# Optimization experiments

Measured on AMD Instinct MI355X. Metric: run time of the kernel, lower is better.

## Reference

```python
import jax, jax.numpy as jnp
import numpy as np

N = 100000        # num_nodes
W_IN = 256        # input feature dim
W_OUT = 64        # args.node_dim
C = 2             # args.num_channels
T = 4             # num_edge_type
E = 800000        # edges per edge type
NUM_CLASS = 4
M = 20000         # number of target nodes
BETA = 0.5        # args.beta


def setup_inputs() -> dict:
    key = jax.random.key(0)
    ks = jax.random.split(key, 10)
    X = jax.random.normal(ks[0], (N, W_IN), dtype=jnp.float32)
    edge_index = jax.random.randint(ks[1], (T, 2, E), 0, N)
    edge_value = jax.random.uniform(ks[2], (T, E), dtype=jnp.float32)
    target_x = jax.random.randint(ks[3], (M,), 0, N)
    target = jax.random.randint(ks[4], (M,), 0, NUM_CLASS)
    # learned params
    Ws = jax.random.normal(ks[5], (C, W_IN, W_OUT), dtype=jnp.float32) * 0.05   # GCNConv weights
    conv_weight = jax.random.normal(ks[6], (C, T), dtype=jnp.float32) * 0.1     # FastGTConv.weight
    linear1_W = jax.random.normal(ks[7], (W_OUT, W_OUT * C), dtype=jnp.float32) * 0.05
    linear1_b = jnp.zeros((W_OUT,), dtype=jnp.float32)
    lin_W = jax.random.normal(ks[8], (NUM_CLASS, W_OUT), dtype=jnp.float32) * 0.05
    lin_b = jnp.zeros((NUM_CLASS,), dtype=jnp.float32)
    return dict(X=X, edge_value=edge_value, Ws=Ws, conv_weight=conv_weight,
                linear1_W=linear1_W, linear1_b=linear1_b, lin_W=lin_W, lin_b=lin_b,
                edge_index=edge_index, target_x=target_x, target=target)


def reference(X, edge_value, Ws, conv_weight, linear1_W, linear1_b, lin_W, lin_b,
              edge_index, target_x, target):
    # FastGTConv: softmax over edge types per channel
    filt = jax.nn.softmax(conv_weight, axis=1)            # [C, T]
    rows = edge_index[:, 0, :].reshape(-1)                # [T*E]
    cols = edge_index[:, 1, :].reshape(-1)                # [T*E]
    # X_ = H = [X @ W_c for each channel]
    X_ = jnp.einsum('nd,cdo->cno', X, Ws)                 # [C, N, W_OUT]
    outs = []
    for c in range(C):
        # concat+coalesce(add) then spmm == scatter-add of weighted messages
        vals = (edge_value * filt[c][:, None]).reshape(-1)       # [T*E]
        msgs = vals[:, None] * X_[c][cols]                        # [T*E, W_OUT]
        Hc = jax.ops.segment_sum(msgs, rows, num_segments=N)      # [N, W_OUT]
        outs.append(jax.nn.relu(BETA * X_[c] + (1.0 - BETA) * Hc))
    H_ = jnp.concatenate(outs, axis=1)                    # [N, C*W_OUT]
    H_ = jax.nn.relu(H_ @ linear1_W.T + linear1_b)        # [N, W_OUT]
    y = H_[target_x] @ lin_W.T + lin_b                    # [M, NUM_CLASS]
    logp = jax.nn.log_softmax(y, axis=-1)
    loss = -jnp.mean(jnp.take_along_axis(logp, target[:, None], axis=1))
    return loss, y
```

## Files before the change

### kernel.cpp

```cpp
#include <hip/hip_runtime.h>

#define N_NODES 100000
#define W_INF   256
#define W_OUTF  64
#define C_CH    2
#define T_ET    4
#define E_EDGE  800000
#define NUM_CLS 4
#define M_TGT   20000
#define BETA    0.5f
#define MAXDEG  96

typedef __attribute__((ext_vector_type(8))) short bf16x8;
typedef __attribute__((ext_vector_type(4))) float floatx4;

__device__ inline short f2bf(float f) {
    unsigned u = __builtin_bit_cast(unsigned, f);
    u += 0x7FFF + ((u >> 16) & 1);
    return (short)(u >> 16);
}
__device__ inline float bflo(unsigned q) { return __builtin_bit_cast(float, q << 16); }
__device__ inline float bfhi(unsigned q) { return __builtin_bit_cast(float, q & 0xFFFF0000u); }
__device__ __forceinline__ float rlane(float v, int k) {
    return __builtin_bit_cast(float,
        __builtin_amdgcn_readlane(__builtin_bit_cast(int, v), k));
}

__global__ void setup_kernel(const float* __restrict__ Ws,
                             const float* __restrict__ conv_weight,
                             const int* __restrict__ target_x,
                             short* __restrict__ Bt, float* __restrict__ filt,
                             int* __restrict__ rid, int* __restrict__ nrows,
                             float* __restrict__ out) {
    int i = blockIdx.x * 256 + threadIdx.x;
    if (i == 0) { nrows[0] = 0; out[0] = 0.f; }
    if (i < C_CH) {
        int c = i;
        float mx = -1e30f;
        for (int t = 0; t < T_ET; t++) mx = fmaxf(mx, conv_weight[c * T_ET + t]);
        float e[T_ET];
        float s = 0.f;
        for (int t = 0; t < T_ET; t++) { e[t] = expf(conv_weight[c * T_ET + t] - mx); s += e[t]; }
        for (int t = 0; t < T_ET; t++) filt[c * T_ET + t] = e[t] / s;
    }
    if (i < C_CH * W_OUTF * W_INF) {
        int co = i >> 8, k = i & 255;
        int c = co >> 6, o = co & 63;
        Bt[i] = f2bf(Ws[((size_t)c * W_INF + k) * W_OUTF + o]);
    }
    if (i < M_TGT) rid[target_x[i]] = -2;
}

__global__ void compact_kernel(int* __restrict__ rid, int* __restrict__ row_list,
                               int* __restrict__ nrows, int* __restrict__ counts) {
    int n = blockIdx.x * blockDim.x + threadIdx.x;
    if (n < M_TGT) counts[n] = 0;
    int lane = threadIdx.x & 63;
    bool flag = (n < N_NODES) && (rid[n] == -2);
    unsigned long long mask = __ballot(flag);
    int base = 0;
    if (lane == 0 && mask) base = atomicAdd(nrows, __popcll(mask));
    base = __shfl(base, 0);
    if (flag) {
        int id = base + __popcll(mask & ((1ULL << lane) - 1ULL));
        rid[n] = id;
        row_list[id] = n;
    }
}

#define GMT  64
#define BLDA2 136
#define GEMM_NB  ((N_NODES + GMT - 1) / GMT)
#define BUILD_BX ((E_EDGE / 8 + 255) / 256)
#define BUILD_TOT (BUILD_BX * T_ET)
__global__ __launch_bounds__(256, 4)
void fused_gemm_build(const float* __restrict__ X, const short* __restrict__ Bt,
                      short* __restrict__ Xp,
                      const int* __restrict__ edge_index,
                      const float* __restrict__ edge_value,
                      const float* __restrict__ filt,
                      const int* __restrict__ rid,
                      int* __restrict__ counts,
                      unsigned long long* __restrict__ records) {
    __shared__ short Bl[64][BLDA2];
    int tid = threadIdx.x;
    int bx = blockIdx.x;
    if ((bx & 1) == 0) {
        int g = bx >> 1;
        if (g >= GEMM_NB) return;
        int w = tid >> 6, lane = tid & 63;
        int quad = lane >> 4, l15 = lane & 15;
        int m0 = g * GMT + w * 16;
        int arow = m0 + l15;
        if (arow >= N_NODES) arow = N_NODES - 1;
        const float* xrow = X + (size_t)arow * W_INF;
        floatx4 acc[C_CH][4] = {};
        #pragma unroll 1
        for (int kh = 0; kh < 2; kh++) {
            bf16x8 af[4];
            #pragma unroll
            for (int kc = 0; kc < 4; kc++) {
                int kb = kh * 128 + kc * 32 + quad * 8;
                float4 v0 = *(const float4*)&xrow[kb];
                float4 v1 = *(const float4*)&xrow[kb + 4];
                af[kc][0] = f2bf(v0.x); af[kc][1] = f2bf(v0.y);
                af[kc][2] = f2bf(v0.z); af[kc][3] = f2bf(v0.w);
                af[kc][4] = f2bf(v1.x); af[kc][5] = f2bf(v1.y);
                af[kc][6] = f2bf(v1.z); af[kc][7] = f2bf(v1.w);
            }
            #pragma unroll
            for (int c = 0; c < C_CH; c++) {
                if (kh | c) __syncthreads();
                #pragma unroll
                for (int l = 0; l < 4; l++) {
                    int idx = tid + l * 256;
                    int r = idx >> 4;
                    int kp = (idx & 15) * 8;
                    *(bf16x8*)&Bl[r][kp] =
                        *(const bf16x8*)&Bt[(size_t)(c * 64 + r) * W_INF + kh * 128 + kp];
                }
                __syncthreads();
                #pragma unroll
                for (int kc = 0; kc < 4; kc++) {
                    int kb = kc * 32 + quad * 8;
                    #pragma unroll
                    for (int nt = 0; nt < 4; nt++) {
                        bf16x8 b = *(bf16x8*)&Bl[nt * 16 + l15][kb];
                        acc[c][nt] =
                            __builtin_amdgcn_mfma_f32_16x16x32_bf16(af[kc], b, acc[c][nt], 0, 0, 0);
                    }
                }
            }
        }
        #pragma unroll
        for (int nt = 0; nt < 4; nt++) {
            int o = nt * 16 + l15;
            #pragma unroll
            for (int r = 0; r < 4; r++) {
                int m = m0 + quad * 4 + r;
                if (m < N_NODES) {
                    unsigned pk = (unsigned)(unsigned short)f2bf(acc[0][nt][r])
                                | ((unsigned)(unsigned short)f2bf(acc[1][nt][r]) << 16);
                    *(unsigned*)&Xp[(size_t)m * (C_CH * W_OUTF) + o * 2] = pk;
                }
            }
        }
    } else {
        int bb = bx >> 1;
        if (bb >= BUILD_TOT) return;
        int t = bb / BUILD_BX;
        int i = (bb - t * BUILD_BX) * 256 + tid;
        if (i >= E_EDGE / 8) return;
        float f0t = filt[t] * (1.0f - BETA);
        float f1t = filt[T_ET + t] * (1.0f - BETA);
        int e = i * 8;
        const int*   rbase = &edge_index[(size_t)(t * 2 + 0) * E_EDGE + e];
        const int*   cbase = &edge_index[(size_t)(t * 2 + 1) * E_EDGE + e];
        const float* vbase = &edge_value[(size_t)t * E_EDGE + e];
        int4   r4a = *(const int4*)  &rbase[0], r4b = *(const int4*)  &rbase[4];
        int4   c4a = *(const int4*)  &cbase[0], c4b = *(const int4*)  &cbase[4];
        float4 v4a = *(const float4*)&vbase[0], v4b = *(const float4*)&vbase[4];
        int rows[8] = {r4a.x, r4a.y, r4a.z, r4a.w, r4b.x, r4b.y, r4b.z, r4b.w};
        int cols[8] = {c4a.x, c4a.y, c4a.z, c4a.w, c4b.x, c4b.y, c4b.z, c4b.w};
        float evv[8] = {v4a.x, v4a.y, v4a.z, v4a.w, v4b.x, v4b.y, v4b.z, v4b.w};
        int ids[8];
        #pragma unroll
        for (int j = 0; j < 8; j++) ids[j] = rid[rows[j]];
        #pragma unroll
        for (int j = 0; j < 8; j++) {
            if (ids[j] >= 0) {
                int p = atomicAdd(&counts[ids[j]], 1);
                if (p < MAXDEG) {
                    unsigned ef = (unsigned)(unsigned short)f2bf(evv[j] * f0t)
                                | ((unsigned)(unsigned short)f2bf(evv[j] * f1t) << 16);
                    unsigned long long rec =
                        (unsigned long long)(unsigned)cols[j] |
                        ((unsigned long long)ef << 32);
                    records[(size_t)ids[j] * MAXDEG + p] = rec;
                }
            }
        }
    }
}

#define GROWS 8
__device__ __forceinline__ void process_row(
    int n, int cnt, unsigned long long rl, unsigned long long rh,
    const unsigned* __restrict__ xb, const float (*w1s)[W_OUTF],
    float bias, int lane,
    float lw0, float lw1, float lw2, float lw3,
    float lb0, float lb1, float lb2, float lb3,
    float4* __restrict__ yv, int b)
{
    unsigned rl_lo = (unsigned)rl, rl_hi = (unsigned)(rl >> 32);
    unsigned rh_lo = (unsigned)rh, rh_hi = (unsigned)(rh >> 32);
    float a0 = 0.f, a1 = 0.f, a0b = 0.f, a1b = 0.f;
    int nb = (cnt + 15) & ~15;
    for (int p = 0; p < nb; p += 16) {
        unsigned blo = (p < 64) ? rl_lo : rh_lo;
        unsigned bhi = (p < 64) ? rl_hi : rh_hi;
        int poff = (p < 64) ? p : p - 64;
        unsigned klo[16], khi[16], q[16];
        #pragma unroll
        for (int j = 0; j < 16; j++) {
            klo[j] = __shfl(blo, poff + j);
            khi[j] = __shfl(bhi, poff + j);
        }
        #pragma unroll
        for (int j = 0; j < 16; j++)
            q[j] = xb[(size_t)(klo[j] & 0xFFFFF) * 64];
        #pragma unroll
        for (int j = 0; j < 16; j += 2) {
            a0  += bflo(khi[j])     * bflo(q[j]);
            a1  += bfhi(khi[j])     * bfhi(q[j]);
            a0b += bflo(khi[j + 1]) * bflo(q[j + 1]);
            a1b += bfhi(khi[j + 1]) * bfhi(q[j + 1]);
        }
    }
    a0 += a0b; a1 += a1b;
    unsigned qn = xb[(size_t)n * 64];
    float hc0 = fmaxf(BETA * bflo(qn) + a0, 0.f);
    float hc1 = fmaxf(BETA * bfhi(qn) + a1, 0.f);
    float s0 = bias, s1 = 0.f, s2 = 0.f, s3 = 0.f;
    #pragma unroll
    for (int k = 0; k < W_OUTF; k += 4) {
        s0 += rlane(hc0, k)     * w1s[k][lane ^ (k & 31)];
        s1 += rlane(hc0, k + 1) * w1s[k + 1][lane ^ ((k + 1) & 31)];
        s2 += rlane(hc0, k + 2) * w1s[k + 2][lane ^ ((k + 2) & 31)];
        s3 += rlane(hc0, k + 3) * w1s[k + 3][lane ^ ((k + 3) & 31)];
    }
    #pragma unroll
    for (int k = 0; k < W_OUTF; k += 4) {
        s0 += rlane(hc1, k)     * w1s[W_OUTF + k][lane ^ (k & 31)];
        s1 += rlane(hc1, k + 1) * w1s[W_OUTF + k + 1][lane ^ ((k + 1) & 31)];
        s2 += rlane(hc1, k + 2) * w1s[W_OUTF + k + 2][lane ^ ((k + 2) & 31)];
        s3 += rlane(hc1, k + 3) * w1s[W_OUTF + k + 3][lane ^ ((k + 3) & 31)];
    }
    float h2 = fmaxf((s0 + s1) + (s2 + s3), 0.f);
    float p0 = lw0 * h2, p1 = lw1 * h2, p2 = lw2 * h2, p3 = lw3 * h2;
    #pragma unroll
    for (int off = 32; off > 0; off >>= 1) {
        p0 += __shfl_xor(p0, off);
        p1 += __shfl_xor(p1, off);
        p2 += __shfl_xor(p2, off);
        p3 += __shfl_xor(p3, off);
    }
    if (lane == 0)
        yv[b] = make_float4(p0 + lb0, p1 + lb1, p2 + lb2, p3 + lb3);
}

__global__ void gather_kernel(const int* __restrict__ row_list,
                              const int* __restrict__ counts,
                              const unsigned long long* __restrict__ records,
                              const short* __restrict__ Xp,
                              const float* __restrict__ W1,
                              const float* __restrict__ b1,
                              const float* __restrict__ linW,
                              const float* __restrict__ linb,
                              float4* __restrict__ yv,
                              const int* __restrict__ nrows_ptr) {
    __shared__ float w1s[C_CH * W_OUTF][W_OUTF];
    int tid = threadIdx.x;
    for (int i = tid; i < W_OUTF * C_CH * W_OUTF; i += 256) {
        int o = i >> 7, k = i & 127;
        w1s[k][o ^ (k & 31)] = W1[i];
    }
    __syncthreads();
    int w = tid >> 6, lane = tid & 63;
    int nrows = nrows_ptr[0];
    float bias = b1[lane];
    float lw0 = linW[0 * W_OUTF + lane], lw1 = linW[1 * W_OUTF + lane];
    float lw2 = linW[2 * W_OUTF + lane], lw3 = linW[3 * W_OUTF + lane];
    float lb0 = linb[0], lb1 = linb[1], lb2 = linb[2], lb3 = linb[3];
    const unsigned* xb = (const unsigned*)Xp + lane;

    int b0 = blockIdx.x * GROWS + w;
    int b1r = b0 + 4;
    bool v0 = b0 < nrows, v1 = b1r < nrows;
    int n0 = 0, c0 = 0, n1 = 0, c1 = 0;
    unsigned long long rl0 = 0, rh0 = 0, rl1 = 0, rh1 = 0;
    if (v0) {
        n0 = row_list[b0];
        c0 = counts[b0]; if (c0 > MAXDEG) c0 = MAXDEG;
        const unsigned long long* rec = records + (size_t)b0 * MAXDEG;
        rl0 = (lane < c0)      ? rec[lane]      : 0ULL;
        rh0 = (lane + 64 < c0) ? rec[lane + 64] : 0ULL;
    }
    if (v1) {
        n1 = row_list[b1r];
        c1 = counts[b1r]; if (c1 > MAXDEG) c1 = MAXDEG;
        const unsigned long long* rec = records + (size_t)b1r * MAXDEG;
        rl1 = (lane < c1)      ? rec[lane]      : 0ULL;
        rh1 = (lane + 64 < c1) ? rec[lane + 64] : 0ULL;
    }
    if (v0) process_row(n0, c0, rl0, rh0, xb, w1s, bias, lane,
                        lw0, lw1, lw2, lw3, lb0, lb1, lb2, lb3, yv, b0);
    if (v1) process_row(n1, c1, rl1, rh1, xb, w1s, bias, lane,
                        lw0, lw1, lw2, lw3, lb0, lb1, lb2, lb3, yv, b1r);
}

__global__ void loss_kernel(const float4* __restrict__ yv,
                            const int* __restrict__ rid,
                            const int* __restrict__ target_x,
                            const int* __restrict__ target,
                            float* __restrict__ out) {
    __shared__ float loss_s[4];
    int tid = threadIdx.x;
    int wave = tid >> 6, lane = tid & 63;
    int m = blockIdx.x * 256 + tid;
    float l = 0.f;
    if (m < M_TGT) {
        int id = rid[target_x[m]];
        float4 y = yv[id];
        *(float4*)&out[1 + (size_t)m * NUM_CLS] = y;
        float mx = fmaxf(fmaxf(y.x, y.y), fmaxf(y.z, y.w));
        float s = expf(y.x - mx) + expf(y.y - mx) + expf(y.z - mx) + expf(y.w - mx);
        float lse = mx + logf(s);
        int tg = target[m];
        float ytg = (tg == 0) ? y.x : (tg == 1) ? y.y : (tg == 2) ? y.z : y.w;
        l = lse - ytg;
    }
    #pragma unroll
    for (int off = 32; off > 0; off >>= 1) l += __shfl_xor(l, off);
    if (lane == 0) loss_s[wave] = l;
    __syncthreads();
    if (tid == 0) {
        float L = loss_s[0] + loss_s[1] + loss_s[2] + loss_s[3];
        atomicAdd(&out[0], L * (1.0f / (float)M_TGT));
    }
}

extern "C" void kernel_launch(void* const* d_in, const int* in_sizes, int n_in,
                              void* d_out, int out_size, void* d_ws, size_t ws_size,
                              hipStream_t stream) {
    const float* X           = (const float*)d_in[0];
    const float* edge_value  = (const float*)d_in[1];
    const float* Ws          = (const float*)d_in[2];
    const float* conv_weight = (const float*)d_in[3];
    const float* linear1_W   = (const float*)d_in[4];
    const float* linear1_b   = (const float*)d_in[5];
    const float* lin_W       = (const float*)d_in[6];
    const float* lin_b       = (const float*)d_in[7];
    const int*   edge_index  = (const int*)d_in[8];
    const int*   target_x    = (const int*)d_in[9];
    const int*   target      = (const int*)d_in[10];
    float* out = (float*)d_out;

    char* ws = (char*)d_ws;
    size_t off = 0;
    float* filt  = (float*)(ws + off); off += 256;
    size_t xbytes = (size_t)N_NODES * C_CH * W_OUTF * sizeof(short);
    short* Xp    = (short*)(ws + off); off += xbytes;
    float4* yv   = (float4*)(ws + off); off += (size_t)M_TGT * sizeof(float4);
    unsigned long long* records = (unsigned long long*)(ws + off);
    off += (size_t)M_TGT * MAXDEG * sizeof(unsigned long long);
    short* Bt    = (short*)(ws + off); off += (size_t)C_CH * W_OUTF * W_INF * sizeof(short);
    int*   rid   = (int*)  (ws + off); off += (size_t)N_NODES * sizeof(int);
    int*   row_list = (int*)(ws + off); off += (size_t)M_TGT * sizeof(int);
    int*   counts   = (int*)(ws + off); off += (size_t)M_TGT * sizeof(int);
    int*   nrows    = (int*)(ws + off); off += 256;

    hipMemsetAsync(rid, 0xFF, (size_t)N_NODES * sizeof(int), stream);

    setup_kernel<<<128, 256, 0, stream>>>(Ws, conv_weight, target_x, Bt, filt, rid, nrows, out);
    compact_kernel<<<(N_NODES + 255) / 256, 256, 0, stream>>>(rid, row_list, nrows, counts);
    fused_gemm_build<<<2 * BUILD_TOT, 256, 0, stream>>>(
        X, Bt, Xp, edge_index, edge_value, filt, rid, counts, records);
    gather_kernel<<<(M_TGT + GROWS - 1) / GROWS, 256, 0, stream>>>(
        row_list, counts, records, Xp, linear1_W, linear1_b,
        lin_W, lin_b, yv, nrows);
    loss_kernel<<<(M_TGT + 255) / 256, 256, 0, stream>>>(yv, rid, target_x, target, out);
}
```

Before: 283.7 us.

## Use split-bf16 MFMA for linear1 in gather kernel, 16 rows per block

The gather kernel no longer stages the full fp32 linear1 weight in shared memory per block or does the per-row readlane matmul. Instead it writes the aggregated hidden rows to LDS as high/low bf16 pairs and runs a 16-row block through MFMA 16x16x32 with three-term split precision, using W1 pre-split in the setup kernel. This removes the per-block 32KB weight load and scalar readlane dot products, but leaves only one wave doing the matmul and adds a block barrier. The GEMM LDS padding constant is also changed.

```diff
diff --git a/kernel.cpp b/kernel.cpp
--- a/kernel.cpp
+++ b/kernel.cpp
@@ -13,6 +13,7 @@
 
 typedef __attribute__((ext_vector_type(8))) short bf16x8;
 typedef __attribute__((ext_vector_type(4))) float floatx4;
+typedef unsigned long long ull;
 
 __device__ inline short f2bf(float f) {
     unsigned u = __builtin_bit_cast(unsigned, f);
@@ -21,15 +22,19 @@
 }
 __device__ inline float bflo(unsigned q) { return __builtin_bit_cast(float, q << 16); }
 __device__ inline float bfhi(unsigned q) { return __builtin_bit_cast(float, q & 0xFFFF0000u); }
-__device__ __forceinline__ float rlane(float v, int k) {
-    return __builtin_bit_cast(float,
-        __builtin_amdgcn_readlane(__builtin_bit_cast(int, v), k));
+__device__ inline void bfsplit(float v, short& h, short& l) {
+    unsigned u = __builtin_bit_cast(unsigned, v) & 0xFFFF0000u;
+    h = (short)(u >> 16);
+    l = f2bf(v - __builtin_bit_cast(float, u));
 }
 
 __global__ void setup_kernel(const float* __restrict__ Ws,
                              const float* __restrict__ conv_weight,
+                             const float* __restrict__ W1,
                              const int* __restrict__ target_x,
-                             short* __restrict__ Bt, float* __restrict__ filt,
+                             short* __restrict__ Bt,
+                             short* __restrict__ w1h, short* __restrict__ w1l,
+                             float* __restrict__ filt,
                              int* __restrict__ rid, int* __restrict__ nrows,
                              float* __restrict__ out) {
     int i = blockIdx.x * 256 + threadIdx.x;
@@ -47,6 +52,11 @@
         int co = i >> 8, k = i & 255;
         int c = co >> 6, o = co & 63;
         Bt[i] = f2bf(Ws[((size_t)c * W_INF + k) * W_OUTF + o]);
+    }
+    if (i < C_CH * W_OUTF * W_OUTF) {
+        short h, l;
+        bfsplit(W1[i], h, l);
+        w1h[i] = h; w1l[i] = l;
     }
     if (i < M_TGT) rid[target_x[i]] = -2;
 }
@@ -69,7 +79,7 @@
 }
 
 #define GMT  64
-#define BLDA2 136
+#define BLDA2 152
 #define GEMM_NB  ((N_NODES + GMT - 1) / GMT)
 #define BUILD_BX ((E_EDGE / 8 + 255) / 256)
 #define BUILD_TOT (BUILD_BX * T_ET)
@@ -183,120 +193,140 @@
     }
 }
 
-#define GROWS 8
-__device__ __forceinline__ void process_row(
-    int n, int cnt, unsigned long long rl, unsigned long long rh,
-    const unsigned* __restrict__ xb, const float (*w1s)[W_OUTF],
-    float bias, int lane,
-    float lw0, float lw1, float lw2, float lw3,
-    float lb0, float lb1, float lb2, float lb3,
-    float4* __restrict__ yv, int b)
-{
-    unsigned rl_lo = (unsigned)rl, rl_hi = (unsigned)(rl >> 32);
-    unsigned rh_lo = (unsigned)rh, rh_hi = (unsigned)(rh >> 32);
-    float a0 = 0.f, a1 = 0.f, a0b = 0.f, a1b = 0.f;
-    int nb = (cnt + 15) & ~15;
-    for (int p = 0; p < nb; p += 16) {
-        unsigned blo = (p < 64) ? rl_lo : rh_lo;
-        unsigned bhi = (p < 64) ? rl_hi : rh_hi;
-        int poff = (p < 64) ? p : p - 64;
-        unsigned klo[16], khi[16], q[16];
-        #pragma unroll
-        for (int j = 0; j < 16; j++) {
-            klo[j] = __shfl(blo, poff + j);
-            khi[j] = __shfl(bhi, poff + j);
-        }
-        #pragma unroll
-        for (int j = 0; j < 16; j++)
-            q[j] = xb[(size_t)(klo[j] & 0xFFFFF) * 64];
-        #pragma unroll
-        for (int j = 0; j < 16; j += 2) {
-            a0  += bflo(khi[j])     * bflo(q[j]);
-            a1  += bfhi(khi[j])     * bfhi(q[j]);
-            a0b += bflo(khi[j + 1]) * bflo(q[j + 1]);
-            a1b += bfhi(khi[j + 1]) * bfhi(q[j + 1]);
-        }
-    }
-    a0 += a0b; a1 += a1b;
-    unsigned qn = xb[(size_t)n * 64];
-    float hc0 = fmaxf(BETA * bflo(qn) + a0, 0.f);
-    float hc1 = fmaxf(BETA * bfhi(qn) + a1, 0.f);
-    float s0 = bias, s1 = 0.f, s2 = 0.f, s3 = 0.f;
+#define GROWS2 16
+__global__ __launch_bounds__(256)
+void gather_kernel(const int* __restrict__ row_list,
+                   const int* __restrict__ counts,
+                   const unsigned long long* __restrict__ records,
+                   const short* __restrict__ Xp,
+                   const short* __restrict__ w1h, const short* __restrict__ w1l,
+                   const float* __restrict__ b1,
+                   const float* __restrict__ linW,
+                   const float* __restrict__ linb,
+                   float4* __restrict__ yv,
+                   const int* __restrict__ nrows_ptr) {
+    __shared__ short hcH[GROWS2][136];
+    __shared__ short hcL[GROWS2][136];
+    __shared__ float linS[NUM_CLS][W_OUTF];
+    int tid = threadIdx.x;
+    int nrows = nrows_ptr[0];
+    int blockStart = blockIdx.x * GROWS2;
+    if (blockStart >= nrows) return;
+    if (tid < NUM_CLS * W_OUTF) linS[tid >> 6][tid & 63] = linW[tid];
+    int w = tid >> 6, lane = tid & 63;
+    const unsigned* xb = (const unsigned*)Xp + lane;
+
+    int base = blockStart + w * 4;
+    int nn[4], cc[4];
+    ull rl[4], rh[4];
     #pragma unroll
-    for (int k = 0; k < W_OUTF; k += 4) {
-        s0 += rlane(hc0, k)     * w1s[k][lane ^ (k & 31)];
-        s1 += rlane(hc0, k + 1) * w1s[k + 1][lane ^ ((k + 1) & 31)];
-        s2 += rlane(hc0, k + 2) * w1s[k + 2][lane ^ ((k + 2) & 31)];
-        s3 += rlane(hc0, k + 3) * w1s[k + 3][lane ^ ((k + 3) & 31)];
+    for (int r = 0; r < 4; r++) {
+        int b = base + r;
+        nn[r] = 0; cc[r] = 0; rl[r] = 0; rh[r] = 0;
+        if (b < nrows) {
+            nn[r] = row_list[b];
+            int c = counts[b]; if (c > MAXDEG) c = MAXDEG;
+            cc[r] = c;
+            const ull* rec = records + (size_t)b * MAXDEG;
+            rl[r] = (lane < c)      ? rec[lane]      : 0ULL;
+            rh[r] = (lane + 64 < c) ? rec[lane + 64] : 0ULL;
+        }
     }
     #pragma unroll
-    for (int k = 0; k < W_OUTF; k += 4) {
-        s0 += rlane(hc1, k)     * w1s[W_OUTF + k][lane ^ (k & 31)];
-        s1 += rlane(hc1, k + 1) * w1s[W_OUTF + k + 1][lane ^ ((k + 1) & 31)];
-        s2 += rlane(hc1, k + 2) * w1s[W_OUTF + k + 2][lane ^ ((k + 2) & 31)];
-        s3 += rlane(hc1, k + 3) * w1s[W_OUTF + k + 3][lane ^ ((k + 3) & 31)];
-    }
-    float h2 = fmaxf((s0 + s1) + (s2 + s3), 0.f);
-    float p0 = lw0 * h2, p1 = lw1 * h2, p2 = lw2 * h2, p3 = lw3 * h2;
-    #pragma unroll
-    for (int off = 32; off > 0; off >>= 1) {
-        p0 += __shfl_xor(p0, off);
-        p1 += __shfl_xor(p1, off);
-        p2 += __shfl_xor(p2, off);
-        p3 += __shfl_xor(p3, off);
-    }
-    if (lane == 0)
-        yv[b] = make_float4(p0 + lb0, p1 + lb1, p2 + lb2, p3 + lb3);
-}
-
-__global__ void gather_kernel(const int* __restrict__ row_list,
-                              const int* __restrict__ counts,
-                              const unsigned long long* __restrict__ records,
-                              const short* __restrict__ Xp,
-                              const float* __restrict__ W1,
-                              const float* __restrict__ b1,
-                              const float* __restrict__ linW,
-                              const float* __restrict__ linb,
-                              float4* __restrict__ yv,
-                              const int* __restrict__ nrows_ptr) {
-    __shared__ float w1s[C_CH * W_OUTF][W_OUTF];
-    int tid = threadIdx.x;
-    for (int i = tid; i < W_OUTF * C_CH * W_OUTF; i += 256) {
-        int o = i >> 7, k = i & 127;
-        w1s[k][o ^ (k & 31)] = W1[i];
+    for (int r = 0; r < 4; r++) {
+        if (base + r < nrows) {
+            unsigned rl_lo = (unsigned)rl[r], rl_hi = (unsigned)(rl[r] >> 32);
+            unsigned rh_lo = (unsigned)rh[r], rh_hi = (unsigned)(rh[r] >> 32);
+            float a0 = 0.f, a1 = 0.f, a0b = 0.f, a1b = 0.f;
+            int nb = (cc[r] + 15) & ~15;
+            for (int p = 0; p < nb; p += 16) {
+                unsigned blo = (p < 64) ? rl_lo : rh_lo;
+                unsigned bhi = (p < 64) ? rl_hi : rh_hi;
+                int poff = (p < 64) ? p : p - 64;
+                unsigned klo[16], khi[16], q[16];
+                #pragma unroll
+                for (int j = 0; j < 16; j++) {
+                    klo[j] = __shfl(blo, poff + j);
+                    khi[j] = __shfl(bhi, poff + j);
+                }
+                #pragma unroll
+                for (int j = 0; j < 16; j++)
+                    q[j] = xb[(size_t)(klo[j] & 0xFFFFF) * 64];
+                #pragma unroll
+                for (int j = 0; j < 16; j += 2) {
+                    a0  += bflo(khi[j])     * bflo(q[j]);
+                    a1  += bfhi(khi[j])     * bfhi(q[j]);
+                    a0b += bflo(khi[j + 1]) * bflo(q[j + 1]);
+                    a1b += bfhi(khi[j + 1]) * bfhi(q[j + 1]);
+                }
+            }
+            a0 += a0b; a1 += a1b;
+            unsigned qn = xb[(size_t)nn[r] * 64];
+            float hc0 = fmaxf(BETA * bflo(qn) + a0, 0.f);
+            float hc1 = fmaxf(BETA * bfhi(qn) + a1, 0.f);
+            short h, l;
+            bfsplit(hc0, h, l);
+            hcH[w * 4 + r][lane] = h;  hcL[w * 4 + r][lane] = l;
+            bfsplit(hc1, h, l);
+            hcH[w * 4 + r][64 + lane] = h;  hcL[w * 4 + r][64 + lane] = l;
+        }
     }
     __syncthreads();
-    int w = tid >> 6, lane = tid & 63;
-    int nrows = nrows_ptr[0];
-    float bias = b1[lane];
-    float lw0 = linW[0 * W_OUTF + lane], lw1 = linW[1 * W_OUTF + lane];
-    float lw2 = linW[2 * W_OUTF + lane], lw3 = linW[3 * W_OUTF + lane];
-    float lb0 = linb[0], lb1 = linb[1], lb2 = linb[2], lb3 = linb[3];
-    const unsigned* xb = (const unsigned*)Xp + lane;
-
-    int b0 = blockIdx.x * GROWS + w;
-    int b1r = b0 + 4;
-    bool v0 = b0 < nrows, v1 = b1r < nrows;
-    int n0 = 0, c0 = 0, n1 = 0, c1 = 0;
-    unsigned long long rl0 = 0, rh0 = 0, rl1 = 0, rh1 = 0;
-    if (v0) {
-        n0 = row_list[b0];
-        c0 = counts[b0]; if (c0 > MAXDEG) c0 = MAXDEG;
-        const unsigned long long* rec = records + (size_t)b0 * MAXDEG;
-        rl0 = (lane < c0)      ? rec[lane]      : 0ULL;
-        rh0 = (lane + 64 < c0) ? rec[lane + 64] : 0ULL;
-    }
-    if (v1) {
-        n1 = row_list[b1r];
-        c1 = counts[b1r]; if (c1 > MAXDEG) c1 = MAXDEG;
-        const unsigned long long* rec = records + (size_t)b1r * MAXDEG;
-        rl1 = (lane < c1)      ? rec[lane]      : 0ULL;
-        rh1 = (lane + 64 < c1) ? rec[lane + 64] : 0ULL;
-    }
-    if (v0) process_row(n0, c0, rl0, rh0, xb, w1s, bias, lane,
-                        lw0, lw1, lw2, lw3, lb0, lb1, lb2, lb3, yv, b0);
-    if (v1) process_row(n1, c1, rl1, rh1, xb, w1s, bias, lane,
-                        lw0, lw1, lw2, lw3, lb0, lb1, lb2, lb3, yv, b1r);
+
+    if (w == 0) {
+        int quad = lane >> 4, l15 = lane & 15;
+        floatx4 dacc[4] = {};
+        #pragma unroll
+        for (int s = 0; s < 4; s++) {
+            bf16x8 aH = *(bf16x8*)&hcH[l15][quad * 8 + s * 32];
+            bf16x8 aL = *(bf16x8*)&hcL[l15][quad * 8 + s * 32];
+            #pragma unroll
+            for (int nt = 0; nt < 4; nt++) {
+                size_t wof = (size_t)(l15 + nt * 16) * 128 + quad * 8 + s * 32;
+                bf16x8 bH = *(const bf16x8*)&w1h[wof];
+                bf16x8 bL = *(const bf16x8*)&w1l[wof];
+                dacc[nt] = __builtin_amdgcn_mfma_f32_16x16x32_bf16(aH, bH, dacc[nt], 0, 0, 0);
+                dacc[nt] = __builtin_amdgcn_mfma_f32_16x16x32_bf16(aL, bH, dacc[nt], 0, 0, 0);
+                dacc[nt] = __builtin_amdgcn_mfma_f32_16x16x32_bf16(aH, bL, dacc[nt], 0, 0, 0);
+            }
+        }
+        float h2v[4][4];
+        #pragma unroll
+        for (int nt = 0; nt < 4; nt++) {
+            float bv = b1[l15 + nt * 16];
+            #pragma unroll
+            for (int j = 0; j < 4; j++)
+                h2v[nt][j] = fmaxf(dacc[nt][j] + bv, 0.f);
+        }
+        float pc[4][4];
+        #pragma unroll
+        for (int c = 0; c < 4; c++) {
+            float lw0 = linS[c][l15], lw1 = linS[c][l15 + 16];
+            float lw2 = linS[c][l15 + 32], lw3 = linS[c][l15 + 48];
+            #pragma unroll
+            for (int j = 0; j < 4; j++)
+                pc[c][j] = h2v[0][j] * lw0 + h2v[1][j] * lw1
+                         + h2v[2][j] * lw2 + h2v[3][j] * lw3;
+        }
+        #pragma unroll
+        for (int off = 1; off < 16; off <<= 1) {
+            #pragma unroll
+            for (int c = 0; c < 4; c++)
+                #pragma unroll
+                for (int j = 0; j < 4; j++)
+                    pc[c][j] += __shfl_xor(pc[c][j], off);
+        }
+        if (l15 == 0) {
+            float lb0 = linb[0], lb1 = linb[1], lb2 = linb[2], lb3 = linb[3];
+            #pragma unroll
+            for (int j = 0; j < 4; j++) {
+                int row = blockStart + quad * 4 + j;
+                if (row < nrows)
+                    yv[row] = make_float4(pc[0][j] + lb0, pc[1][j] + lb1,
+                                          pc[2][j] + lb2, pc[3][j] + lb3);
+            }
+        }
+    }
 }
 
 __global__ void loss_kernel(const float4* __restrict__ yv,
@@ -355,6 +385,8 @@
     unsigned long long* records = (unsigned long long*)(ws + off);
     off += (size_t)M_TGT * MAXDEG * sizeof(unsigned long long);
     short* Bt    = (short*)(ws + off); off += (size_t)C_CH * W_OUTF * W_INF * sizeof(short);
+    short* w1h   = (short*)(ws + off); off += (size_t)C_CH * W_OUTF * W_OUTF * sizeof(short);
+    short* w1l   = (short*)(ws + off); off += (size_t)C_CH * W_OUTF * W_OUTF * sizeof(short);
     int*   rid   = (int*)  (ws + off); off += (size_t)N_NODES * sizeof(int);
     int*   row_list = (int*)(ws + off); off += (size_t)M_TGT * sizeof(int);
     int*   counts   = (int*)(ws + off); off += (size_t)M_TGT * sizeof(int);
@@ -362,12 +394,13 @@
 
     hipMemsetAsync(rid, 0xFF, (size_t)N_NODES * sizeof(int), stream);
 
-    setup_kernel<<<128, 256, 0, stream>>>(Ws, conv_weight, target_x, Bt, filt, rid, nrows, out);
+    setup_kernel<<<128, 256, 0, stream>>>(Ws, conv_weight, linear1_W, target_x,
+                                          Bt, w1h, w1l, filt, rid, nrows, out);
     compact_kernel<<<(N_NODES + 255) / 256, 256, 0, stream>>>(rid, row_list, nrows, counts);
     fused_gemm_build<<<2 * BUILD_TOT, 256, 0, stream>>>(
         X, Bt, Xp, edge_index, edge_value, filt, rid, counts, records);
-    gather_kernel<<<(M_TGT + GROWS - 1) / GROWS, 256, 0, stream>>>(
-        row_list, counts, records, Xp, linear1_W, linear1_b,
+    gather_kernel<<<(M_TGT + GROWS2 - 1) / GROWS2, 256, 0, stream>>>(
+        row_list, counts, records, Xp, w1h, w1l, linear1_b,
         lin_W, lin_b, yv, nrows);
     loss_kernel<<<(M_TGT + 255) / 256, 256, 0, stream>>>(yv, rid, target_x, target, out);
 }
```

Measured after the change: 278.3 us. About the same (-1.9%).
